# Kernel tuning notes

Hardware: AMD Instinct MI355X
Metric: run time of the kernel (lower is better)

The kernel has to match this reference:

```python
import jax, jax.numpy as jnp
import numpy as np
from jax import lax

R = 3.0            # search_range (std of random-search perturbation)
THRESH = 1.05      # UPDATE_MULTIPLIER_THRESHOLD


def _score(coords, corr):
    """Bilinear sample each leading-dim element's own corr map at its coord.
    coords: (..., 2) with [..., 0]=x (width), [..., 1]=y (height)
    corr:   (..., H, W) with matching leading dims. Zero padding outside.
    Returns (...,) scores. Matches RAFT bilinear_sampler + grid_sample(align_corners=True)."""
    H, W = corr.shape[-2], corr.shape[-1]
    lead = coords.shape[:-1]
    c = coords.reshape(-1, 2)
    v = corr.reshape(-1, H, W)
    n = jnp.arange(v.shape[0])
    x, y = c[:, 0], c[:, 1]
    x0 = jnp.floor(x)
    y0 = jnp.floor(y)
    wx1 = x - x0
    wy1 = y - y0

    def tap(xi, yi, w):
        valid = (xi >= 0) & (xi <= W - 1) & (yi >= 0) & (yi <= H - 1)
        xc = jnp.clip(xi, 0, W - 1).astype(jnp.int32)
        yc = jnp.clip(yi, 0, H - 1).astype(jnp.int32)
        return w * jnp.where(valid, v[n, yc, xc], 0.0)

    s = (tap(x0, y0, (1 - wx1) * (1 - wy1))
         + tap(x0 + 1, y0, wx1 * (1 - wy1))
         + tap(x0, y0 + 1, (1 - wx1) * wy1)
         + tap(x0 + 1, y0 + 1, wx1 * wy1))
    return s.reshape(lead)


def _clamp(c, H, W):
    return jnp.stack([jnp.clip(c[..., 0], 0.0, W - 1.0),
                      jnp.clip(c[..., 1], 0.0, H - 1.0)], axis=-1)


def _propagate(coords, corr, dy, dx):
    """PatchMatch propagation sweep in direction (dy, dx) (equivalent of the
    custom matching_prop CUDA kernel). Sequential raster sweep: each pixel
    adopts top-neighbor coords + (0,dy) or left-neighbor coords + (dx,0) if
    the bilinear-sampled correlation score improves.
    coords: (B,H,W,2), corr: (B,H,W,H,W)."""
    B, H, W = coords.shape[:3]
    c, cm = coords, corr
    if dy < 0:
        c = jnp.flip(c, 1)
        cm = jnp.flip(cm, 1)
    if dx < 0:
        c = jnp.flip(c, 2)
        cm = jnp.flip(cm, 2)
    rows = jnp.moveaxis(c, 1, 0)        # (H,B,W,2)
    corr_rows = jnp.moveaxis(cm, 1, 0)  # (H,B,W,H,W)
    voff = jnp.array([0.0, float(dy)], dtype=c.dtype)
    hoff = jnp.array([float(dx), 0.0], dtype=c.dtype)

    def col_step(prev, xs):
        cpx, corr_px, spx, j = xs       # (B,2), (B,H,W), (B,), ()
        hc = _clamp(prev + hoff, H, W)
        hs = _score(hc, corr_px)
        u = (hs > spx) & (j > 0)
        new = jnp.where(u[:, None], hc, cpx)
        return new, new

    def row_step(prev_row, xs):
        cur, corr_row, i = xs           # (B,W,2), (B,W,H,W), ()
        cs = _score(cur, corr_row)      # (B,W)
        vc = _clamp(prev_row + voff, H, W)
        vs = _score(vc, corr_row)
        u = (vs > cs) & (i > 0)
        cur = jnp.where(u[..., None], vc, cur)
        cs = jnp.where(u, vs, cs)
        xs_cols = (jnp.moveaxis(cur, 1, 0), jnp.moveaxis(corr_row, 1, 0),
                   cs.T, jnp.arange(W))
        _, out = lax.scan(col_step, jnp.zeros((B, 2), cur.dtype), xs_cols)
        out = jnp.moveaxis(out, 0, 1)   # (B,W,2)
        return out, out

    _, res = lax.scan(row_step, jnp.zeros((B, W, 2), c.dtype),
                      (rows, corr_rows, jnp.arange(H)))
    res = jnp.moveaxis(res, 0, 1)       # (B,H,W,2)
    if dx < 0:
        res = jnp.flip(res, 2)
    if dy < 0:
        res = jnp.flip(res, 1)
    return res


def _random_search(coords, corr, eps):
    """Faithful port of __random_search (including sequential boundary
    assignments that overwrite BOTH coordinate channels, as in the source)."""
    H, W = coords.shape[1], coords.shape[2]
    new = coords + R * eps                 # torch.normal(coords, r)
    new = jnp.maximum(new, 0.0)            # new_coords[new_coords < 0] = 0
    new = jnp.where((new[..., 0] >= H)[..., None], float(H - 1), new)
    new = jnp.where((new[..., 1] >= W)[..., None], float(W - 1), new)
    old_s = _score(coords, corr)
    new_s = _score(new, corr)
    upd = new_s > THRESH * old_s
    return jnp.where(upd[..., None], new, coords)


def reference(raw_coords, corr_map, noise):
    # raw_coords: (B,2,H,W), corr_map: (B,H,W,H,W), noise: (3,B,H,W,2)
    coords = jnp.transpose(raw_coords, (0, 2, 3, 1))  # (B,H,W,2)
    dirs = ((1, 1), (-1, -1), (-1, 1), (1, -1))
    for k, (dy, dx) in enumerate(dirs):
        coords = _propagate(coords, corr_map, dy, dx)
        if k < 3:
            coords = _random_search(coords, corr_map, noise[k])
    return jnp.transpose(coords, (0, 3, 1, 2))        # (B,2,H,W)


def setup_inputs() -> dict:
    key = jax.random.key(0)
    k1, k2, k3 = jax.random.split(key, 3)
    B, H, W = 2, 64, 64
    raw_coords = jax.random.uniform(k1, (B, 2, H, W), dtype=jnp.float32) * (W - 1.0)
    corr_map = jax.random.uniform(k2, (B, H, W, H, W), dtype=jnp.float32)
    noise = jax.random.normal(k3, (3, B, H, W, 2), dtype=jnp.float32)
    return {"raw_coords": raw_coords, "corr_map": corr_map, "noise": noise}
```

## Files before the change

### kernel.cpp

```cpp
#include <hip/hip_runtime.h>


__device__ __forceinline__ float clamp63(float v) {
    return fminf(fmaxf(v, 0.0f), 63.0f);
}

__device__ __forceinline__ float bsample(const float* __restrict__ m, float x, float y) {
    float x0f = floorf(x), y0f = floorf(y);
    float wx1 = __fsub_rn(x, x0f);
    float wy1 = __fsub_rn(y, y0f);
    float wx0 = __fsub_rn(1.0f, wx1);
    float wy0 = __fsub_rn(1.0f, wy1);
    int x0 = (int)x0f, y0 = (int)y0f;
    int x1 = x0 + 1, y1 = y0 + 1;
    const float* row0 = m + y0 * 64;
    float v00 = row0[x0];
    float v10 = (x1 <= 63) ? row0[x1] : 0.0f;
    float v01 = (y1 <= 63) ? m[y1 * 64 + x0] : 0.0f;
    float v11 = ((x1 <= 63) && (y1 <= 63)) ? m[y1 * 64 + x1] : 0.0f;
    float t0 = __fmul_rn(__fmul_rn(wx0, wy0), v00);
    float t1 = __fmul_rn(__fmul_rn(wx1, wy0), v10);
    float t2 = __fmul_rn(__fmul_rn(wx0, wy1), v01);
    float t3 = __fmul_rn(__fmul_rn(wx1, wy1), v11);
    return __fadd_rn(__fadd_rn(__fadd_rn(t0, t1), t2), t3);
}

__global__ __launch_bounds__(1024) void MatchingPropagator_65180423685702_kernel(
        const float* __restrict__ raw,
        const float* __restrict__ corr,
        const float* __restrict__ noise,
        float* __restrict__ out) {
    const int blk = blockIdx.x;

    if (blk >= 2) {
        const size_t total4 = (size_t)2 * 64 * 64 * 4096 / 4;
        const float4* c4 = (const float4*)corr;
        const size_t stride = (size_t)(gridDim.x - 2) * blockDim.x;
        float acc = 0.0f;
        for (size_t idx = (size_t)(blk - 2) * blockDim.x + threadIdx.x;
             idx < total4; idx += stride) {
            float4 v = c4[idx];
            acc += v.x + v.y + v.z + v.w;
        }
        asm volatile("" :: "v"(acc));
        return;
    }

    const int b = blk;
    const float* __restrict__ corrb = corr + (size_t)b * 64 * 64 * 4096;
    const int tid = threadIdx.x;

    __shared__ float lx[4096];
    __shared__ float ly[4096];
    __shared__ float ls[4096];

    for (int p = tid; p < 4096; p += blockDim.x) {
        float x = raw[(size_t)b * 8192 + p];
        float y = raw[(size_t)b * 8192 + 4096 + p];
        lx[p] = x; ly[p] = y;
        ls[p] = bsample(corrb + (size_t)p * 4096, x, y);
    }
    __syncthreads();

    const int dys[4] = {1, -1, -1, 1};
    const int dxs[4] = {1, -1, 1, -1};

#pragma unroll
    for (int k = 0; k < 4; ++k) {
        const int dy = dys[k], dx = dxs[k];
        if (tid < 64) {
            const int r = tid;
            const int i = (dy > 0) ? r : 63 - r;
            float cx = 0.0f, cy = 0.0f;
            for (int d = 0; d < 127; ++d) {
                float vnx = __shfl_up(cx, 1);
                float vny = __shfl_up(cy, 1);
                const int c = d - r;
                if (c >= 0 && c < 64) {
                    const int j = (dx > 0) ? c : 63 - c;
                    const int p = i * 64 + j;
                    const float* m = corrb + (size_t)p * 4096;
                    float px = lx[p], py = ly[p], ps = ls[p];
                    float vcx = clamp63(vnx);
                    float vcy = clamp63(__fadd_rn(vny, (float)dy));
                    float hcx = clamp63(__fadd_rn(cx, (float)dx));
                    float hcy = clamp63(cy);
                    float vs = bsample(m, vcx, vcy);
                    float hs = bsample(m, hcx, hcy);
                    bool uv = (vs > ps) && (r > 0);
                    float ux = uv ? vcx : px;
                    float uy = uv ? vcy : py;
                    float us = uv ? vs : ps;
                    bool uh = (hs > us) && (c > 0);
                    cx = uh ? hcx : ux;
                    cy = uh ? hcy : uy;
                    float fs = uh ? hs : us;
                    lx[p] = cx; ly[p] = cy; ls[p] = fs;
                }
            }
        }
        __syncthreads();

        if (k < 3) {
            const float* nz = noise + ((size_t)k * 2 + b) * 8192;
            for (int p = tid; p < 4096; p += blockDim.x) {
                float x = lx[p], y = ly[p], s = ls[p];
                float ex = nz[p * 2 + 0], ey = nz[p * 2 + 1];
                float nx = fmaxf(__fadd_rn(x, __fmul_rn(3.0f, ex)), 0.0f);
                float ny = fmaxf(__fadd_rn(y, __fmul_rn(3.0f, ey)), 0.0f);
                if (nx >= 64.0f) { nx = 63.0f; ny = 63.0f; }
                if (ny >= 64.0f) { nx = 63.0f; ny = 63.0f; }
                float ns = bsample(corrb + (size_t)p * 4096, nx, ny);
                if (ns > __fmul_rn(1.05f, s)) {
                    lx[p] = nx; ly[p] = ny; ls[p] = ns;
                }
            }
            __syncthreads();
        }
    }

    for (int p = tid; p < 4096; p += blockDim.x) {
        out[(size_t)b * 8192 + p] = lx[p];
        out[(size_t)b * 8192 + 4096 + p] = ly[p];
    }
}

extern "C" void kernel_launch(void* const* d_in, const int* in_sizes, int n_in,
                              void* d_out, int out_size, void* d_ws, size_t ws_size,
                              hipStream_t stream) {
    const float* raw   = (const float*)d_in[0];
    const float* corr  = (const float*)d_in[1];
    const float* noise = (const float*)d_in[2];
    float* out = (float*)d_out;
    (void)in_sizes; (void)n_in; (void)out_size; (void)d_ws; (void)ws_size;
    MatchingPropagator_65180423685702_kernel<<<256, 1024, 0, stream>>>(raw, corr, noise, out);
}
```

Baseline: 394.4 us.

## Drop cache-warming helper blocks and issue all bilinear gathers unconditionally

Removes the 254 extra blocks that streamed the whole correlation volume to warm the cache, so only the two per-batch blocks launch. In the serial wavefront sweep, the two bilinear samples are inlined, with clamped indices so all eight corner loads issue without branches and can overlap. Out-of-range taps are zeroed after loading. The risk is that the sweep's dependent gathers no longer hit data prefetched into the last-level cache, which raises their latency.

```diff
diff --git a/kernel.cpp b/kernel.cpp
--- a/kernel.cpp
+++ b/kernel.cpp
@@ -13,11 +13,16 @@
     float wy0 = __fsub_rn(1.0f, wy1);
     int x0 = (int)x0f, y0 = (int)y0f;
     int x1 = x0 + 1, y1 = y0 + 1;
+    int x1c = min(x1, 63), y1c = min(y1, 63);
     const float* row0 = m + y0 * 64;
+    const float* row1 = m + y1c * 64;
     float v00 = row0[x0];
-    float v10 = (x1 <= 63) ? row0[x1] : 0.0f;
-    float v01 = (y1 <= 63) ? m[y1 * 64 + x0] : 0.0f;
-    float v11 = ((x1 <= 63) && (y1 <= 63)) ? m[y1 * 64 + x1] : 0.0f;
+    float v10 = row0[x1c];
+    float v01 = row1[x0];
+    float v11 = row1[x1c];
+    v10 = (x1 <= 63) ? v10 : 0.0f;
+    v01 = (y1 <= 63) ? v01 : 0.0f;
+    v11 = ((x1 <= 63) && (y1 <= 63)) ? v11 : 0.0f;
     float t0 = __fmul_rn(__fmul_rn(wx0, wy0), v00);
     float t1 = __fmul_rn(__fmul_rn(wx1, wy0), v10);
     float t2 = __fmul_rn(__fmul_rn(wx0, wy1), v01);
@@ -25,28 +30,12 @@
     return __fadd_rn(__fadd_rn(__fadd_rn(t0, t1), t2), t3);
 }
 
-__global__ __launch_bounds__(1024) void MatchingPropagator_65180423685702_kernel(
+__global__ __launch_bounds__(1024, 1) void MatchingPropagator_65180423685702_kernel(
         const float* __restrict__ raw,
         const float* __restrict__ corr,
         const float* __restrict__ noise,
         float* __restrict__ out) {
-    const int blk = blockIdx.x;
-
-    if (blk >= 2) {
-        const size_t total4 = (size_t)2 * 64 * 64 * 4096 / 4;
-        const float4* c4 = (const float4*)corr;
-        const size_t stride = (size_t)(gridDim.x - 2) * blockDim.x;
-        float acc = 0.0f;
-        for (size_t idx = (size_t)(blk - 2) * blockDim.x + threadIdx.x;
-             idx < total4; idx += stride) {
-            float4 v = c4[idx];
-            acc += v.x + v.y + v.z + v.w;
-        }
-        asm volatile("" :: "v"(acc));
-        return;
-    }
-
-    const int b = blk;
+    const int b = blockIdx.x;
     const float* __restrict__ corrb = corr + (size_t)b * 64 * 64 * 4096;
     const int tid = threadIdx.x;
 
@@ -68,9 +57,11 @@
 #pragma unroll
     for (int k = 0; k < 4; ++k) {
         const int dy = dys[k], dx = dxs[k];
+        const float fdy = (float)dy, fdx = (float)dx;
         if (tid < 64) {
             const int r = tid;
             const int i = (dy > 0) ? r : 63 - r;
+            const float* rowbase = corrb + (size_t)i * 64 * 4096;
             float cx = 0.0f, cy = 0.0f;
             for (int d = 0; d < 127; ++d) {
                 float vnx = __shfl_up(cx, 1);
@@ -79,14 +70,52 @@
                 if (c >= 0 && c < 64) {
                     const int j = (dx > 0) ? c : 63 - c;
                     const int p = i * 64 + j;
-                    const float* m = corrb + (size_t)p * 4096;
+                    const float* m = rowbase + (size_t)j * 4096;
                     float px = lx[p], py = ly[p], ps = ls[p];
                     float vcx = clamp63(vnx);
-                    float vcy = clamp63(__fadd_rn(vny, (float)dy));
-                    float hcx = clamp63(__fadd_rn(cx, (float)dx));
+                    float vcy = clamp63(__fadd_rn(vny, fdy));
+                    float hcx = clamp63(__fadd_rn(cx, fdx));
                     float hcy = clamp63(cy);
-                    float vs = bsample(m, vcx, vcy);
-                    float hs = bsample(m, hcx, hcy);
+                    float vx0f = floorf(vcx), vy0f = floorf(vcy);
+                    float hx0f = floorf(hcx), hy0f = floorf(hcy);
+                    int vx0 = (int)vx0f, vy0 = (int)vy0f;
+                    int hx0 = (int)hx0f, hy0 = (int)hy0f;
+                    int vx1 = vx0 + 1, vy1 = vy0 + 1;
+                    int hx1 = hx0 + 1, hy1 = hy0 + 1;
+                    int vx1c = min(vx1, 63), vy1c = min(vy1, 63);
+                    int hx1c = min(hx1, 63), hy1c = min(hy1, 63);
+                    const float* va = m + vy0 * 64;
+                    const float* vb = m + vy1c * 64;
+                    const float* ha = m + hy0 * 64;
+                    const float* hb = m + hy1c * 64;
+                    float a00 = va[vx0];
+                    float a10 = va[vx1c];
+                    float a01 = vb[vx0];
+                    float a11 = vb[vx1c];
+                    float b00 = ha[hx0];
+                    float b10 = ha[hx1c];
+                    float b01 = hb[hx0];
+                    float b11 = hb[hx1c];
+                    float vwx1 = __fsub_rn(vcx, vx0f), vwy1 = __fsub_rn(vcy, vy0f);
+                    float vwx0 = __fsub_rn(1.0f, vwx1), vwy0 = __fsub_rn(1.0f, vwy1);
+                    float hwx1 = __fsub_rn(hcx, hx0f), hwy1 = __fsub_rn(hcy, hy0f);
+                    float hwx0 = __fsub_rn(1.0f, hwx1), hwy0 = __fsub_rn(1.0f, hwy1);
+                    float vw00 = __fmul_rn(vwx0, vwy0), vw10 = __fmul_rn(vwx1, vwy0);
+                    float vw01 = __fmul_rn(vwx0, vwy1), vw11 = __fmul_rn(vwx1, vwy1);
+                    float hw00 = __fmul_rn(hwx0, hwy0), hw10 = __fmul_rn(hwx1, hwy0);
+                    float hw01 = __fmul_rn(hwx0, hwy1), hw11 = __fmul_rn(hwx1, hwy1);
+                    a10 = (vx1 <= 63) ? a10 : 0.0f;
+                    a01 = (vy1 <= 63) ? a01 : 0.0f;
+                    a11 = ((vx1 <= 63) && (vy1 <= 63)) ? a11 : 0.0f;
+                    b10 = (hx1 <= 63) ? b10 : 0.0f;
+                    b01 = (hy1 <= 63) ? b01 : 0.0f;
+                    b11 = ((hx1 <= 63) && (hy1 <= 63)) ? b11 : 0.0f;
+                    float vs = __fadd_rn(__fadd_rn(__fadd_rn(
+                                   __fmul_rn(vw00, a00), __fmul_rn(vw10, a10)),
+                                   __fmul_rn(vw01, a01)), __fmul_rn(vw11, a11));
+                    float hs = __fadd_rn(__fadd_rn(__fadd_rn(
+                                   __fmul_rn(hw00, b00), __fmul_rn(hw10, b10)),
+                                   __fmul_rn(hw01, b01)), __fmul_rn(hw11, b11));
                     bool uv = (vs > ps) && (r > 0);
                     float ux = uv ? vcx : px;
                     float uy = uv ? vcy : py;
@@ -133,5 +162,5 @@
     const float* noise = (const float*)d_in[2];
     float* out = (float*)d_out;
     (void)in_sizes; (void)n_in; (void)out_size; (void)d_ws; (void)ws_size;
-    MatchingPropagator_65180423685702_kernel<<<256, 1024, 0, stream>>>(raw, corr, noise, out);
+    MatchingPropagator_65180423685702_kernel<<<2, 1024, 0, stream>>>(raw, corr, noise, out);
 }
```

Result: faster. 356.1 us (-9.7%).

## Speculatively prefetch all candidate taps one step ahead in propagation wavefront

Applied to the files above, without the earlier changes.

The propagation wavefront now prefetches bilinear taps for all three possible outcomes (keep, vertical, horizontal) of the previous step for both candidates. The next step then only selects among register values, taking global-memory latency off the serial dependency chain. Tap loads are also merged into paired 8-byte reads. The extra 254 blocks that streamed the whole corr tensor (apparently to warm the cache) are removed, and the launch shrinks to 2 blocks. In exchange each step issues many more loads and uses more registers, and the cache warming is lost.

```diff
diff --git a/kernel.cpp b/kernel.cpp
--- a/kernel.cpp
+++ b/kernel.cpp
@@ -1,8 +1,15 @@
 #include <hip/hip_runtime.h>
 
+
+struct __attribute__((packed, aligned(4))) f2u { float x, y; };
 
 __device__ __forceinline__ float clamp63(float v) {
     return fminf(fmaxf(v, 0.0f), 63.0f);
+}
+
+__device__ __forceinline__ float sel3f(int s, float a0, float a1, float a2) {
+    float r = (s == 1) ? a1 : a0;
+    return (s == 2) ? a2 : r;
 }
 
 __device__ __forceinline__ float bsample(const float* __restrict__ m, float x, float y) {
@@ -13,11 +20,16 @@
     float wy0 = __fsub_rn(1.0f, wy1);
     int x0 = (int)x0f, y0 = (int)y0f;
     int x1 = x0 + 1, y1 = y0 + 1;
-    const float* row0 = m + y0 * 64;
-    float v00 = row0[x0];
-    float v10 = (x1 <= 63) ? row0[x1] : 0.0f;
-    float v01 = (y1 <= 63) ? m[y1 * 64 + x0] : 0.0f;
-    float v11 = ((x1 <= 63) && (y1 <= 63)) ? m[y1 * 64 + x1] : 0.0f;
+    int y1c = min(y1, 63);
+    int bx = min(x0, 62);
+    f2u p0 = *(const f2u*)(m + y0 * 64 + bx);
+    f2u p1 = *(const f2u*)(m + y1c * 64 + bx);
+    bool hi = (x0 > 62);
+    float v00 = hi ? p0.y : p0.x;
+    float v10 = (x1 <= 63) ? p0.y : 0.0f;
+    float v01 = hi ? p1.y : p1.x;
+    v01 = (y1 <= 63) ? v01 : 0.0f;
+    float v11 = ((x1 <= 63) && (y1 <= 63)) ? p1.y : 0.0f;
     float t0 = __fmul_rn(__fmul_rn(wx0, wy0), v00);
     float t1 = __fmul_rn(__fmul_rn(wx1, wy0), v10);
     float t2 = __fmul_rn(__fmul_rn(wx0, wy1), v01);
@@ -25,28 +37,50 @@
     return __fadd_rn(__fadd_rn(__fadd_rn(t0, t1), t2), t3);
 }
 
-__global__ __launch_bounds__(1024) void MatchingPropagator_65180423685702_kernel(
+__device__ __forceinline__ float score_taps(float x, float y, f2u p0, f2u p1) {
+    float x0f = floorf(x), y0f = floorf(y);
+    float wx1 = __fsub_rn(x, x0f);
+    float wy1 = __fsub_rn(y, y0f);
+    float wx0 = __fsub_rn(1.0f, wx1);
+    float wy0 = __fsub_rn(1.0f, wy1);
+    int x0 = (int)x0f, y0 = (int)y0f;
+    int x1 = x0 + 1, y1 = y0 + 1;
+    bool hi = (x0 > 62);
+    float v00 = hi ? p0.y : p0.x;
+    float v10 = (x1 <= 63) ? p0.y : 0.0f;
+    float v01 = hi ? p1.y : p1.x;
+    v01 = (y1 <= 63) ? v01 : 0.0f;
+    float v11 = ((x1 <= 63) && (y1 <= 63)) ? p1.y : 0.0f;
+    float t0 = __fmul_rn(__fmul_rn(wx0, wy0), v00);
+    float t1 = __fmul_rn(__fmul_rn(wx1, wy0), v10);
+    float t2 = __fmul_rn(__fmul_rn(wx0, wy1), v01);
+    float t3 = __fmul_rn(__fmul_rn(wx1, wy1), v11);
+    return __fadd_rn(__fadd_rn(__fadd_rn(t0, t1), t2), t3);
+}
+
+__device__ __forceinline__ void tapload(const float* __restrict__ m, float x, float y,
+                                        f2u& A, f2u& B) {
+    int x0 = (int)floorf(x);
+    int y0 = (int)floorf(y);
+    int bx = min(x0, 62);
+    int y1c = min(y0 + 1, 63);
+    A = *(const f2u*)(m + y0 * 64 + bx);
+    B = *(const f2u*)(m + y1c * 64 + bx);
+}
+
+struct Bank {
+    float hx0, hy0, hx1, hy1, hx2, hy2;
+    float vx0, vy0, vx1, vy1, vx2, vy2;
+    f2u hA0, hB0, hA1, hB1, hA2, hB2;
+    f2u vA0, vB0, vA1, vB1, vA2, vB2;
+};
+
+__global__ __launch_bounds__(1024, 1) void MatchingPropagator_65180423685702_kernel(
         const float* __restrict__ raw,
         const float* __restrict__ corr,
         const float* __restrict__ noise,
         float* __restrict__ out) {
-    const int blk = blockIdx.x;
-
-    if (blk >= 2) {
-        const size_t total4 = (size_t)2 * 64 * 64 * 4096 / 4;
-        const float4* c4 = (const float4*)corr;
-        const size_t stride = (size_t)(gridDim.x - 2) * blockDim.x;
-        float acc = 0.0f;
-        for (size_t idx = (size_t)(blk - 2) * blockDim.x + threadIdx.x;
-             idx < total4; idx += stride) {
-            float4 v = c4[idx];
-            acc += v.x + v.y + v.z + v.w;
-        }
-        asm volatile("" :: "v"(acc));
-        return;
-    }
-
-    const int b = blk;
+    const int b = blockIdx.x;
     const float* __restrict__ corrb = corr + (size_t)b * 64 * 64 * 4096;
     const int tid = threadIdx.x;
 
@@ -68,35 +102,81 @@
 #pragma unroll
     for (int k = 0; k < 4; ++k) {
         const int dy = dys[k], dx = dxs[k];
+        const float fdy = (float)dy, fdx = (float)dx;
+        const bool dxpos = (dx > 0);
+
         if (tid < 64) {
             const int r = tid;
             const int i = (dy > 0) ? r : 63 - r;
-            float cx = 0.0f, cy = 0.0f;
-            for (int d = 0; d < 127; ++d) {
-                float vnx = __shfl_up(cx, 1);
-                float vny = __shfl_up(cy, 1);
+            const float* rowbase = corrb + (size_t)i * 64 * 4096;
+            int sme = 0;
+            Bank bA = {}, bB = {};
+
+            auto prefetch = [&](int cnext, float kx0, float ky0, float kx1, float ky1,
+                                float kx2, float ky2, Bank& o) {
+                float nx0 = __shfl_up(kx0, 1), ny0 = __shfl_up(ky0, 1);
+                float nx1 = __shfl_up(kx1, 1), ny1 = __shfl_up(ky1, 1);
+                float nx2 = __shfl_up(kx2, 1), ny2 = __shfl_up(ky2, 1);
+                o.hx0 = clamp63(__fadd_rn(kx0, fdx)); o.hy0 = clamp63(ky0);
+                o.hx1 = clamp63(__fadd_rn(kx1, fdx)); o.hy1 = clamp63(ky1);
+                o.hx2 = clamp63(__fadd_rn(kx2, fdx)); o.hy2 = clamp63(ky2);
+                o.vx0 = clamp63(nx0); o.vy0 = clamp63(__fadd_rn(ny0, fdy));
+                o.vx1 = clamp63(nx1); o.vy1 = clamp63(__fadd_rn(ny1, fdy));
+                o.vx2 = clamp63(nx2); o.vy2 = clamp63(__fadd_rn(ny2, fdy));
+                int cn = min(max(cnext, 0), 63);
+                int jn = dxpos ? cn : 63 - cn;
+                const float* m = rowbase + (size_t)jn * 4096;
+                if ((cnext >= 0) && (cnext < 64)) {
+                    tapload(m, o.hx0, o.hy0, o.hA0, o.hB0);
+                    tapload(m, o.hx1, o.hy1, o.hA1, o.hB1);
+                    tapload(m, o.hx2, o.hy2, o.hA2, o.hB2);
+                    tapload(m, o.vx0, o.vy0, o.vA0, o.vB0);
+                    tapload(m, o.vx1, o.vy1, o.vA1, o.vB1);
+                    tapload(m, o.vx2, o.vy2, o.vA2, o.vB2);
+                }
+            };
+
+            auto step = [&](int d, const Bank& in, Bank& o) {
                 const int c = d - r;
-                if (c >= 0 && c < 64) {
-                    const int j = (dx > 0) ? c : 63 - c;
-                    const int p = i * 64 + j;
-                    const float* m = corrb + (size_t)p * 4096;
-                    float px = lx[p], py = ly[p], ps = ls[p];
-                    float vcx = clamp63(vnx);
-                    float vcy = clamp63(__fadd_rn(vny, (float)dy));
-                    float hcx = clamp63(__fadd_rn(cx, (float)dx));
-                    float hcy = clamp63(cy);
-                    float vs = bsample(m, vcx, vcy);
-                    float hs = bsample(m, hcx, hcy);
-                    bool uv = (vs > ps) && (r > 0);
-                    float ux = uv ? vcx : px;
-                    float uy = uv ? vcy : py;
-                    float us = uv ? vs : ps;
-                    bool uh = (hs > us) && (c > 0);
-                    cx = uh ? hcx : ux;
-                    cy = uh ? hcy : uy;
-                    float fs = uh ? hs : us;
-                    lx[p] = cx; ly[p] = cy; ls[p] = fs;
-                }
+                const bool act = (c >= 0) && (c < 64);
+                const int cc = min(max(c, 0), 63);
+                const int j = dxpos ? cc : 63 - cc;
+                const int p = i * 64 + j;
+                int snb = __shfl_up(sme, 1);
+                float px = lx[p], py = ly[p], ps = ls[p];
+                float hcx = sel3f(sme, in.hx0, in.hx1, in.hx2);
+                float hcy = sel3f(sme, in.hy0, in.hy1, in.hy2);
+                float vcx = sel3f(snb, in.vx0, in.vx1, in.vx2);
+                float vcy = sel3f(snb, in.vy0, in.vy1, in.vy2);
+                prefetch(c + 1, px, py, vcx, vcy, hcx, hcy, o);
+                f2u HA, HB, VA, VB;
+                HA.x = sel3f(sme, in.hA0.x, in.hA1.x, in.hA2.x);
+                HA.y = sel3f(sme, in.hA0.y, in.hA1.y, in.hA2.y);
+                HB.x = sel3f(sme, in.hB0.x, in.hB1.x, in.hB2.x);
+                HB.y = sel3f(sme, in.hB0.y, in.hB1.y, in.hB2.y);
+                VA.x = sel3f(snb, in.vA0.x, in.vA1.x, in.vA2.x);
+                VA.y = sel3f(snb, in.vA0.y, in.vA1.y, in.vA2.y);
+                VB.x = sel3f(snb, in.vB0.x, in.vB1.x, in.vB2.x);
+                VB.y = sel3f(snb, in.vB0.y, in.vB1.y, in.vB2.y);
+                float hs = score_taps(hcx, hcy, HA, HB);
+                float vs = score_taps(vcx, vcy, VA, VB);
+                bool uv = (vs > ps) && (r > 0);
+                float ux = uv ? vcx : px;
+                float uy = uv ? vcy : py;
+                float us = uv ? vs : ps;
+                bool uh = (hs > us) && (c > 0);
+                float fx = uh ? hcx : ux;
+                float fy = uh ? hcy : uy;
+                float fs = uh ? hs : us;
+                sme = uh ? 2 : (uv ? 1 : 0);
+                if (act) { lx[p] = fx; ly[p] = fy; ls[p] = fs; }
+            };
+
+            prefetch(0 - r, 0.0f, 0.0f, 0.0f, 0.0f, 0.0f, 0.0f, bA);
+#pragma unroll 1
+            for (int d = 0; d < 128; d += 2) {
+                step(d, bA, bB);
+                step(d + 1, bB, bA);
             }
         }
         __syncthreads();
@@ -133,5 +213,5 @@
     const float* noise = (const float*)d_in[2];
     float* out = (float*)d_out;
     (void)in_sizes; (void)n_in; (void)out_size; (void)d_ws; (void)ws_size;
-    MatchingPropagator_65180423685702_kernel<<<256, 1024, 0, stream>>>(raw, corr, noise, out);
-}
+    MatchingPropagator_65180423685702_kernel<<<2, 1024, 0, stream>>>(raw, corr, noise, out);
+}
```

After: 470.9 us. +19.4%, slower.
